# Performance work log

Hardware: AMD Instinct MI355X
Metric: run time of the kernel (lower is better)

## Reference

```python
import math
import jax, jax.numpy as jnp
from jax import lax
import numpy as np

WH, WW = 5, 9          # window_size
EH, EW = 3, 5          # expand_size = ((ws+1)//2)
NHEAD = 4
D = 512
PK, PS = 4, 4          # pool kernel / stride


def _valid_ind_rolled():
    m = np.ones((4, WH, WW), dtype=np.float32)
    m[0, :WH - EH, :WW - EW] = 0  # tl
    m[1, :WH - EH, EW:] = 0       # tr
    m[2, EH:, :WW - EW] = 0       # bl
    m[3, EH:, EW:] = 0            # br
    return np.nonzero(m.reshape(-1))[0]

VALID_IND = jnp.asarray(_valid_ind_rolled())  # (148,)


def _forward(x, masks, Wq, bq, Wk, bk, Wv, bv, Wp, bp, pool_w, pool_b):
    b, t, h, w, c = x.shape
    hd = c // NHEAD
    n_wh, n_ww = h // WH, w // WW
    n_win = n_wh * n_ww
    S = WH * WW  # tokens per window per frame (45)

    q = x @ Wq + bq
    k = x @ Wk + bk
    v = x @ Wv + bv

    def wp(a):  # window partition -> (b, n_win, nhead, t, S, hd)
        a = a.reshape(b, t, n_wh, WH, n_ww, WW, NHEAD, hd)
        a = a.transpose(0, 2, 4, 6, 1, 3, 5, 7)
        return a.reshape(b, n_win, NHEAD, t, S, hd)

    win_q, win_k, win_v = wp(q), wp(k), wp(v)

    # rolled (shifted) windows, gathered by the static valid-index buffer
    shifts = ((-EH, -EW), (-EH, EW), (EH, -EW), (EH, EW))
    roll_k = jnp.concatenate([wp(jnp.roll(k, s, axis=(2, 3))) for s in shifts], axis=4)[:, :, :, :, VALID_IND]
    roll_v = jnp.concatenate([wp(jnp.roll(v, s, axis=(2, 3))) for s in shifts], axis=4)[:, :, :, :, VALID_IND]

    # pooled global tokens via depthwise conv (kernel 4, stride 4)
    px = lax.conv_general_dilated(
        x.reshape(b * t, h, w, c), pool_w, (PS, PS), 'VALID',
        dimension_numbers=('NHWC', 'HWIO', 'NHWC'), feature_group_count=c) + pool_b
    ph, pw = px.shape[1], px.shape[2]
    P = ph * pw
    px = px.reshape(b, t, P, c)

    def pool_tok(a):  # (b,t,P,c) -> (b,1,nhead,t,P,hd)
        return a.reshape(b, t, P, NHEAD, hd).transpose(0, 3, 1, 2, 4)[:, None]

    pk = jnp.broadcast_to(pool_tok(px @ Wk + bk), (b, n_win, NHEAD, t, P, hd))
    pv = jnp.broadcast_to(pool_tok(px @ Wv + bv), (b, n_win, NHEAD, t, P, hd))

    win_k_full = jnp.concatenate([win_k, roll_k, pk], axis=4)  # (b,n_win,nh,t,K,hd)
    win_v_full = jnp.concatenate([win_v, roll_v, pv], axis=4)
    K = win_k_full.shape[4]

    # window-level mask: max-pool per window per frame, summed over frames, >0
    wmask = masks[..., 0].reshape(b, t, n_wh, WH, n_ww, WW).max(axis=(3, 5))
    wmask = wmask.reshape(b, t, n_win).sum(axis=1) > 0  # (b, n_win)

    scale = 1.0 / math.sqrt(hd)

    # dense spatiotemporal attention (used for masked windows)
    qd = win_q.reshape(b, n_win, NHEAD, t * S, hd)
    kd = win_k_full.reshape(b, n_win, NHEAD, t * K, hd)
    vd = win_v_full.reshape(b, n_win, NHEAD, t * K, hd)
    att_d = jax.nn.softmax(jnp.einsum('bnhqd,bnhkd->bnhqk', qd, kd) * scale, axis=-1)
    y_d = jnp.einsum('bnhqk,bnhkd->bnhqd', att_d, vd).reshape(b, n_win, NHEAD, t, S, hd)

    # per-frame local window attention (used for unmasked windows; keys = first S = window tokens)
    att_l = jax.nn.softmax(jnp.einsum('bnhtqd,bnhtkd->bnhtqk', win_q, win_k) * scale, axis=-1)
    y_l = jnp.einsum('bnhtqk,bnhtkd->bnhtqd', att_l, win_v)

    out = jnp.where(wmask[:, :, None, None, None, None], y_d, y_l)
    out = out.reshape(b, n_wh, n_ww, NHEAD, t, WH, WW, hd)
    out = out.transpose(0, 4, 1, 5, 2, 6, 3, 7).reshape(b, t, h, w, c)
    return out @ Wp + bp


def setup_inputs() -> dict:
    key = jax.random.key(0)
    ks = jax.random.split(key, 8)
    b, t, h, w = 1, 6, 40, 72
    x = jax.random.normal(ks[0], (b, t, h, w, D), dtype=jnp.float32)
    wm = (jax.random.uniform(ks[1], (b, t, h // WH, w // WW)) < 0.3).astype(jnp.float32)
    masks = jnp.repeat(jnp.repeat(wm, WH, axis=2), WW, axis=3)[..., None]
    s = 0.02

    def lin(kk):
        k1, k2 = jax.random.split(kk)
        return (jax.random.normal(k1, (D, D), jnp.float32) * s,
                jax.random.normal(k2, (D,), jnp.float32) * s)

    Wq, bq = lin(ks[2])
    Wk, bk = lin(ks[3])
    Wv, bv = lin(ks[4])
    Wp, bp = lin(ks[5])
    pool_w = jax.random.normal(ks[6], (PK, PK, 1, D), jnp.float32) * s
    pool_b = jax.random.normal(ks[7], (D,), jnp.float32) * s
    return {'x': x, 'masks': masks, 'Wq': Wq, 'bq': bq, 'Wk': Wk, 'bk': bk,
            'Wv': Wv, 'bv': bv, 'Wp': Wp, 'bp': bp, 'pool_w': pool_w, 'pool_b': pool_b}


def reference(x, masks, Wq, bq, Wk, bk, Wv, bv, Wp, bp, pool_w, pool_b):
    return _forward(x, masks, Wq, bq, Wk, bk, Wv, bv, Wp, bp, pool_w, pool_b)
```

## Files before the change

kernel.cpp:

```cpp
#include <hip/hip_runtime.h>

typedef unsigned short u16;
typedef unsigned int u32;
typedef __bf16 bf16x8 __attribute__((ext_vector_type(8)));
typedef float f32x4 __attribute__((ext_vector_type(4)));

#define TT 6
#define NTOK (6*40*72)
#define KTOT 373
#define NKEYS (TT*KTOT)
#define NCH2 35
#define SCALE 0.08838834764831845f
#define K_EXP2 0.12751743f

__device__ __forceinline__ float bf2f(u16 u){ u32 x = ((u32)u) << 16; return __builtin_bit_cast(float, x); }
__device__ __forceinline__ u16 f2bf(float f){ return __builtin_bit_cast(u16, (__bf16)f); }

__device__ __forceinline__ void gload16(const u16* g, u16* l){
  __builtin_amdgcn_global_load_lds(
      (const __attribute__((address_space(1))) void*)g,
      (__attribute__((address_space(3))) void*)l, 16, 0, 0);
}

__global__ __launch_bounds__(256) void convert_x(const float* __restrict__ src, u16* __restrict__ dst, int n4)
{
  int i = blockIdx.x * 256 + threadIdx.x;
  if (i >= n4) return;
  float4 v = *(const float4*)(src + (size_t)i * 4);
  u16 o[4] = {f2bf(v.x), f2bf(v.y), f2bf(v.z), f2bf(v.w)};
  *(uint2*)(dst + (size_t)i * 4) = *(const uint2*)o;
}

__global__ __launch_bounds__(256) void transpose_w(
    const float* __restrict__ w0, const float* __restrict__ w1,
    const float* __restrict__ w2, const float* __restrict__ w3, u16* __restrict__ out)
{
  __shared__ float tile[64][65];
  int m = blockIdx.z;
  const float* src = m == 0 ? w0 : (m == 1 ? w1 : (m == 2 ? w2 : w3));
  int kb = blockIdx.x * 64, nb = blockIdx.y * 64;
  int tid = threadIdx.x;
  int tx = tid & 63, ty = tid >> 6;
#pragma unroll
  for (int i = 0; i < 16; i++)
    tile[ty + 4*i][tx] = src[(size_t)(kb + ty + 4*i) * 512 + nb + tx];
  __syncthreads();
#pragma unroll
  for (int i = 0; i < 16; i++)
    out[m * 262144 + (size_t)(nb + ty + 4*i) * 512 + kb + tx] = f2bf(tile[tx][ty + 4*i]);
}

__global__ __launch_bounds__(256) void gemm_bias(
    const u16* __restrict__ A, const u16* __restrict__ wt,
    const float* __restrict__ b0, const float* __restrict__ b1, const float* __restrict__ b2,
    u16* __restrict__ c0, u16* __restrict__ c1, u16* __restrict__ c2, float* __restrict__ cf,
    int wo0, int wo1, int wo2, int M)
{
  __shared__ __align__(16) u16 sA[128*32];
  __shared__ __align__(16) u16 sB[128*32];
  int z = blockIdx.z;
  const u16* Bt = wt + (size_t)(z == 0 ? wo0 : (z == 1 ? wo1 : wo2)) * 262144;
  const float* bias = z == 0 ? b0 : (z == 1 ? b1 : b2);
  u16* Cout = z == 0 ? c0 : (z == 1 ? c1 : c2);
  int mbase = blockIdx.x * 128, nbase = blockIdx.y * 128;
  int tid = threadIdx.x, lane = tid & 63, wave = tid >> 6;
  int wm = (wave >> 1) * 64, wn = (wave & 1) * 64;
  int quad = lane >> 4, tr = lane & 15;
  int lrow = lane >> 2;
  int seg  = (lane & 3) ^ (lrow & 3);

  const u16* gA[2]; const u16* gB[2];
#pragma unroll
  for (int r = 0; r < 2; r++){
    gA[r] = A  + (size_t)(mbase + wave*32 + r*16 + lrow) * 512 + seg*8;
    gB[r] = Bt + (size_t)(nbase + wave*32 + r*16 + lrow) * 512 + seg*8;
  }
  u16* lA[2]; u16* lB[2];
#pragma unroll
  for (int r = 0; r < 2; r++){
    lA[r] = &sA[(wave*32 + r*16) * 32];
    lB[r] = &sB[(wave*32 + r*16) * 32];
  }

  f32x4 acc[4][4];
#pragma unroll
  for (int i = 0; i < 4; i++)
#pragma unroll
    for (int j = 0; j < 4; j++){ acc[i][j][0]=0.f; acc[i][j][1]=0.f; acc[i][j][2]=0.f; acc[i][j][3]=0.f; }

  int rcol = (quad ^ (tr & 3)) * 8;

  for (int k0 = 0; k0 < 512; k0 += 32){
    if (k0) __syncthreads();
#pragma unroll
    for (int r = 0; r < 2; r++){
      gload16(gA[r] + k0, lA[r]);
      gload16(gB[r] + k0, lB[r]);
    }
    __syncthreads();
    bf16x8 a[4], b[4];
#pragma unroll
    for (int i = 0; i < 4; i++) a[i] = *(const bf16x8*)(&sA[(wm + i*16 + tr)*32 + rcol]);
#pragma unroll
    for (int j = 0; j < 4; j++) b[j] = *(const bf16x8*)(&sB[(wn + j*16 + tr)*32 + rcol]);
#pragma unroll
    for (int i = 0; i < 4; i++)
#pragma unroll
      for (int j = 0; j < 4; j++)
        acc[i][j] = __builtin_amdgcn_mfma_f32_16x16x32_bf16(a[i], b[j], acc[i][j], 0, 0, 0);
  }

#pragma unroll
  for (int j = 0; j < 4; j++){
    int col = nbase + wn + j*16 + tr;
    float bv = bias[col];
#pragma unroll
    for (int i = 0; i < 4; i++)
#pragma unroll
      for (int r2 = 0; r2 < 4; r2++){
        int row = mbase + wm + i*16 + quad*4 + r2;
        if (row < M){
          float val = acc[i][j][r2] + bv;
          if (cf) cf[(size_t)row * 512 + col] = val;
          else    Cout[(size_t)row * 512 + col] = f2bf(val);
        }
      }
  }
}

__global__ __launch_bounds__(256) void pool_conv(
    const float* __restrict__ x, const float* __restrict__ pw,
    const float* __restrict__ pb, u16* __restrict__ px)
{
  int idx = blockIdx.x * 256 + threadIdx.x;
  int c = idx & 511, n = idx >> 9;
  int f = n / 180, rp = n % 180, ph = rp / 18, pwc = rp % 18;
  float acc = pb[c];
#pragma unroll
  for (int i = 0; i < 4; i++)
#pragma unroll
    for (int j = 0; j < 4; j++){
      int hh = ph*4 + i, ww = pwc*4 + j;
      acc += x[((size_t)((f*40 + hh)*72 + ww)) * 512 + c] * pw[(i*4 + j)*512 + c];
    }
  px[idx] = f2bf(acc);
}

__global__ void prep(const float* __restrict__ masks, int* __restrict__ wmask, int* __restrict__ vi)
{
  int tid = threadIdx.x;
  if (tid < 64) wmask[tid] = 0;
  __syncthreads();
  if (tid < 384){
    int f = tid / 64, win = tid & 63;
    int wi = win >> 3, wj = win & 7;
    int flag = 0;
    for (int p = 0; p < 45; p++){
      int hh = wi*5 + p/9, ww = wj*9 + p%9;
      if (masks[(f*40 + hh)*72 + ww] > 0.f) flag = 1;
    }
    if (flag) atomicOr(&wmask[win], 1);
  }
  if (tid == 448){
    int cnt = 0;
    for (int e = 0; e < 180; e++){
      int s = e / 45, pos = e % 45, pr = pos / 9, pc = pos % 9;
      bool inval = (s == 0 && pr < 2 && pc < 4) || (s == 1 && pr < 2 && pc >= 5) ||
                   (s == 2 && pr >= 3 && pc < 4) || (s == 3 && pr >= 3 && pc >= 5);
      if (!inval) vi[cnt++] = e;
    }
  }
}

__global__ __launch_bounds__(256) void build_idx(const int* __restrict__ vip, int* __restrict__ idxTab)
{
  int win = blockIdx.x, wi = win >> 3, wj = win & 7;
  for (int i = threadIdx.x; i < NKEYS; i += 256){
    int f = i / KTOT, slot = i - f * KTOT;
    int idx;
    if (slot < 45){
      int hh = wi*5 + slot/9, ww = wj*9 + slot%9;
      idx = ((f*40 + hh)*72 + ww) * 1024;
    } else if (slot < 193){
      int e = vip[slot - 45];
      int s2 = e / 45, pos = e - s2*45, pr = pos/9, pc = pos - pr*9;
      int hh = wi*5 + pr + ((s2 < 2) ? 3 : -3);
      int ww = wj*9 + pc + ((s2 & 1) ? -5 : 5);
      if (hh < 0) hh += 40; else if (hh >= 40) hh -= 40;
      if (ww < 0) ww += 72; else if (ww >= 72) ww -= 72;
      idx = ((f*40 + hh)*72 + ww) * 1024;
    } else {
      idx = ~((f*180 + (slot - 193)) * 1024);
    }
    idxTab[win * 2240 + i] = idx;
  }
}

__global__ __launch_bounds__(512) void attn_dense(
    const u16* __restrict__ qb, const u16* __restrict__ kb, const u16* __restrict__ vb,
    const u16* __restrict__ pkb, const u16* __restrict__ pvb,
    const int* __restrict__ wmaskp, const int* __restrict__ idxTab,
    u16* __restrict__ yb)
{
  __shared__ __align__(16) u16 sK[64][136];
  __shared__ __align__(16) u16 sVt[128][72];
  __shared__ __align__(16) u16 sP[288][72];
  __shared__ int sIdx[2240];
  __shared__ float sDenX[32];

  int win = blockIdx.x, head = blockIdx.y;
  if (!wmaskp[win]) return;
  int wi = win >> 3, wj = win & 7;
  int tid = threadIdx.x, lane = tid & 63, wave = tid >> 6;
  int quad = lane >> 4, tr = lane & 15;

  if (tid < 32) sDenX[tid] = 0.f;
  {
    const int* g = idxTab + win * 2240;
    for (int i = tid; i < NKEYS; i += 512) sIdx[i] = g[i];
  }

  int mts[3] = {2*wave, 2*wave + 1, 16 + (wave >> 2)};
  bf16x8 qf[3][4];
#pragma unroll
  for (int im = 0; im < 3; im++){
    int row = mts[im]*16 + tr;
    int f = row / 48, r = row - f*48;
    bool vld = r < 45;
    int hh = wi*5 + r/9, ww = wj*9 + r%9;
    const u16* qp = qb + ((size_t)((f*40 + hh)*72 + ww))*512 + head*128;
#pragma unroll
    for (int kt = 0; kt < 4; kt++){
      uint4 v = make_uint4(0,0,0,0);
      if (vld) v = *(const uint4*)(qp + kt*32 + quad*8);
      qf[im][kt] = __builtin_bit_cast(bf16x8, v);
    }
  }

  f32x4 accv[2][8], accx[2];
#pragma unroll
  for (int m = 0; m < 2; m++)
#pragma unroll
    for (int nt = 0; nt < 8; nt++){ accv[m][nt][0]=0.f; accv[m][nt][1]=0.f; accv[m][nt][2]=0.f; accv[m][nt][3]=0.f; }
  accx[0][0]=0.f; accx[0][1]=0.f; accx[0][2]=0.f; accx[0][3]=0.f;
  accx[1][0]=0.f; accx[1][1]=0.f; accx[1][2]=0.f; accx[1][3]=0.f;
  float dacc[2][4], daccx[4];
#pragma unroll
  for (int m = 0; m < 2; m++)
#pragma unroll
    for (int r2 = 0; r2 < 4; r2++) dacc[m][r2] = 0.f;
#pragma unroll
  for (int r2 = 0; r2 < 4; r2++) daccx[r2] = 0.f;

  __syncthreads();

  const char* kb2  = (const char*)kb  + head*256 + (tid & 15)*16;
  const char* pkb2 = (const char*)pkb + head*256 + (tid & 15)*16;
  const char* vb2  = (const char*)vb  + head*256 + (tid >> 6)*16;
  const char* pvb2 = (const char*)pvb + head*256 + (tid >> 6)*16;

  uint4 pfk[2], pfv[2];
  auto pref = [&](int ch){
#pragma unroll
    for (int r = 0; r < 2; r++){ pfk[r] = make_uint4(0,0,0,0); pfv[r] = make_uint4(0,0,0,0); }
    if (ch < NCH2){
      int base = ch * 64;
#pragma unroll
      for (int r = 0; r < 2; r++){
        int jg = base + (tid >> 4) + 32*r;
        if (jg < NKEYS){
          int off = sIdx[jg];
          pfk[r] = *(const uint4*)(off >= 0 ? kb2 + off : pkb2 + ~off);
        }
      }
      int jgv = base + (tid & 63);
      if (jgv < NKEYS){
        int off = sIdx[jgv];
        const char* src = (off >= 0) ? vb2 + off : pvb2 + ~off;
#pragma unroll
        for (int r = 0; r < 2; r++)
          pfv[r] = *(const uint4*)(src + r*128);
      }
    }
  };
  pref(0);

  for (int ch = 0; ch < NCH2; ch++){
    __syncthreads();
#pragma unroll
    for (int r = 0; r < 2; r++)
      *(uint4*)(&sK[(tid >> 4) + 32*r][(tid & 15)*8]) = pfk[r];
    {
      int keyv = tid & 63;
#pragma unroll
      for (int r = 0; r < 2; r++){
        int dgv = (tid >> 6) + 8*r;
        u32 vv[4] = {pfv[r].x, pfv[r].y, pfv[r].z, pfv[r].w};
#pragma unroll
        for (int q2 = 0; q2 < 4; q2++){
          sVt[dgv*8 + q2*2][keyv]     = (u16)(vv[q2] & 0xffff);
          sVt[dgv*8 + q2*2 + 1][keyv] = (u16)(vv[q2] >> 16);
        }
      }
    }
    __syncthreads();
    pref(ch + 1);

#pragma unroll
    for (int nt = 0; nt < 4; nt++){
      bf16x8 bk[4];
#pragma unroll
      for (int kt = 0; kt < 4; kt++) bk[kt] = *(const bf16x8*)(&sK[nt*16 + tr][kt*32 + quad*8]);
      int colg = ch*64 + nt*16 + tr;
      bool vld = colg < NKEYS;
#pragma unroll
      for (int m = 0; m < 2; m++){
        f32x4 s = {0.f, 0.f, 0.f, 0.f};
#pragma unroll
        for (int kt = 0; kt < 4; kt++) s = __builtin_amdgcn_mfma_f32_16x16x32_bf16(qf[m][kt], bk[kt], s, 0, 0, 0);
        int mt = 2*wave + m;
#pragma unroll
        for (int r2 = 0; r2 < 4; r2++){
          float p = vld ? __builtin_amdgcn_exp2f(s[r2] * K_EXP2) : 0.f;
          sP[mt*16 + quad*4 + r2][nt*16 + tr] = f2bf(p);
          dacc[m][r2] += p;
        }
      }
      if (nt == (wave & 3)){
        f32x4 s = {0.f, 0.f, 0.f, 0.f};
#pragma unroll
        for (int kt = 0; kt < 4; kt++) s = __builtin_amdgcn_mfma_f32_16x16x32_bf16(qf[2][kt], bk[kt], s, 0, 0, 0);
        int e = 16 + (wave >> 2);
#pragma unroll
        for (int r2 = 0; r2 < 4; r2++){
          float p = vld ? __builtin_amdgcn_exp2f(s[r2] * K_EXP2) : 0.f;
          sP[e*16 + quad*4 + r2][nt*16 + tr] = f2bf(p);
          daccx[r2] += p;
        }
      }
    }
    __syncthreads();

#pragma unroll
    for (int kt2 = 0; kt2 < 2; kt2++){
      bf16x8 a0 = *(const bf16x8*)(&sP[(2*wave)*16 + tr][kt2*32 + quad*8]);
      bf16x8 a1 = *(const bf16x8*)(&sP[(2*wave + 1)*16 + tr][kt2*32 + quad*8]);
      bf16x8 ax = *(const bf16x8*)(&sP[(16 + (wave >> 2))*16 + tr][kt2*32 + quad*8]);
#pragma unroll
      for (int nt = 0; nt < 8; nt++){
        bf16x8 bv = *(const bf16x8*)(&sVt[nt*16 + tr][kt2*32 + quad*8]);
        accv[0][nt] = __builtin_amdgcn_mfma_f32_16x16x32_bf16(a0, bv, accv[0][nt], 0, 0, 0);
        accv[1][nt] = __builtin_amdgcn_mfma_f32_16x16x32_bf16(a1, bv, accv[1][nt], 0, 0, 0);
      }
      int he0 = (wave & 3)*2;
      bf16x8 bx0 = *(const bf16x8*)(&sVt[he0*16 + tr][kt2*32 + quad*8]);
      bf16x8 bx1 = *(const bf16x8*)(&sVt[(he0+1)*16 + tr][kt2*32 + quad*8]);
      accx[0] = __builtin_amdgcn_mfma_f32_16x16x32_bf16(ax, bx0, accx[0], 0, 0, 0);
      accx[1] = __builtin_amdgcn_mfma_f32_16x16x32_bf16(ax, bx1, accx[1], 0, 0, 0);
    }
  }

#pragma unroll
  for (int r2 = 0; r2 < 4; r2++){
    float d = daccx[r2];
    d += __shfl_xor(d, 1, 64); d += __shfl_xor(d, 2, 64);
    d += __shfl_xor(d, 4, 64); d += __shfl_xor(d, 8, 64);
    if (tr == 0) atomicAdd(&sDenX[(wave >> 2)*16 + quad*4 + r2], d);
  }
  __syncthreads();

#pragma unroll
  for (int m = 0; m < 2; m++){
#pragma unroll
    for (int r2 = 0; r2 < 4; r2++){
      float d = dacc[m][r2];
      d += __shfl_xor(d, 1, 64); d += __shfl_xor(d, 2, 64);
      d += __shfl_xor(d, 4, 64); d += __shfl_xor(d, 8, 64);
      float dinvv = 1.f / d;
      int row = (2*wave + m)*16 + quad*4 + r2;
      int f = row / 48, r = row - f*48;
      if (r < 45){
        int hh = wi*5 + r/9, ww = wj*9 + r%9;
        size_t base = ((size_t)((f*40 + hh)*72 + ww))*512 + head*128;
#pragma unroll
        for (int nt = 0; nt < 8; nt++)
          yb[base + nt*16 + tr] = f2bf(accv[m][nt][r2] * dinvv);
      }
    }
  }
  {
    int e = 16 + (wave >> 2), he0 = (wave & 3)*2;
#pragma unroll
    for (int r2 = 0; r2 < 4; r2++){
      int row = e*16 + quad*4 + r2;
      int f = row / 48, r = row - f*48;
      if (r < 45){
        float dinvv = 1.f / sDenX[(e - 16)*16 + quad*4 + r2];
        int hh = wi*5 + r/9, ww = wj*9 + r%9;
        size_t base = ((size_t)((f*40 + hh)*72 + ww))*512 + head*128;
        yb[base + he0*16 + tr]       = f2bf(accx[0][r2] * dinvv);
        yb[base + (he0 + 1)*16 + tr] = f2bf(accx[1][r2] * dinvv);
      }
    }
  }
}

__device__ __forceinline__ const u16* key_src_local(int slot, int qf, int wi, int wj, int head,
    const u16* __restrict__ tokbuf)
{
  int hh = wi*5 + slot/9, ww = wj*9 + slot%9;
  return tokbuf + ((size_t)((qf*40 + hh)*72 + ww)) * 512 + head * 128;
}

__global__ __launch_bounds__(256) void attn_local(
    const u16* __restrict__ qb, const u16* __restrict__ kb, const u16* __restrict__ vb,
    const int* __restrict__ wmaskp, u16* __restrict__ yb)
{
  __shared__ __align__(16) u16 sQ[48][136];
  __shared__ __align__(16) u16 sK[64][136];
  __shared__ __align__(16) u16 sVt[128][72];
  __shared__ __align__(16) u16 sP[48][72];
  __shared__ float sDen[48];

  int win = blockIdx.x, head = blockIdx.y, qf = blockIdx.z;
  if (wmaskp[win]) return;
  int wi = win >> 3, wj = win & 7;
  int tid = threadIdx.x, lane = tid & 63, wave = tid >> 6;
  int quad = lane >> 4, tr = lane & 15;

  if (tid < 48) sDen[tid] = 0.f;

#pragma unroll
  for (int r = 0; r < 3; r++){
    int u = tid + 256 * r;
    int row = u >> 4, dg = u & 15;
    uint4 val = make_uint4(0,0,0,0);
    if (row < 45){
      int hh = wi*5 + row/9, ww = wj*9 + row%9;
      val = *(const uint4*)(qb + ((size_t)((qf*40 + hh)*72 + ww)) * 512 + head*128 + dg*8);
    }
    *(uint4*)(&sQ[row][dg * 8]) = val;
  }

  const int nkeys = 45;
  f32x4 acc[3][2];
#pragma unroll
  for (int a = 0; a < 3; a++)
#pragma unroll
    for (int b = 0; b < 2; b++){ acc[a][b][0]=0.f; acc[a][b][1]=0.f; acc[a][b][2]=0.f; acc[a][b][3]=0.f; }

#pragma unroll
  for (int r = 0; r < 4; r++){
    int u = tid + 256 * r;
    int key = u >> 4, dg = u & 15;
    uint4 val = make_uint4(0,0,0,0);
    if (key < nkeys) val = *(const uint4*)(key_src_local(key, qf, wi, wj, head, kb) + dg * 8);
    *(uint4*)(&sK[key][dg * 8]) = val;
  }
#pragma unroll
  for (int r = 0; r < 4; r++){
    int u = tid + 256 * r;
    int key = u & 63, dg = u >> 6;
    uint4 val = make_uint4(0,0,0,0);
    if (key < nkeys) val = *(const uint4*)(key_src_local(key, qf, wi, wj, head, vb) + dg * 8);
    u32 vv[4] = {val.x, val.y, val.z, val.w};
#pragma unroll
    for (int q2 = 0; q2 < 4; q2++){
      sVt[dg*8 + q2*2][key]     = (u16)(vv[q2] & 0xffff);
      sVt[dg*8 + q2*2 + 1][key] = (u16)(vv[q2] >> 16);
    }
  }
  __syncthreads();

#pragma unroll
  for (int mt = 0; mt < 3; mt++){
    f32x4 sacc = {0.f, 0.f, 0.f, 0.f};
#pragma unroll
    for (int kt = 0; kt < 4; kt++){
      bf16x8 a = *(const bf16x8*)(&sQ[mt*16 + tr][kt*32 + quad*8]);
      bf16x8 b = *(const bf16x8*)(&sK[wave*16 + tr][kt*32 + quad*8]);
      sacc = __builtin_amdgcn_mfma_f32_16x16x32_bf16(a, b, sacc, 0, 0, 0);
    }
    int colg = wave * 16 + tr;
    float pr4[4];
#pragma unroll
    for (int r2 = 0; r2 < 4; r2++){
      float p = (colg < nkeys) ? __builtin_amdgcn_exp2f(sacc[r2] * K_EXP2) : 0.f;
      sP[mt*16 + quad*4 + r2][wave*16 + tr] = f2bf(p);
      pr4[r2] = p;
    }
#pragma unroll
    for (int r2 = 0; r2 < 4; r2++){
      float ps = pr4[r2];
      ps += __shfl_xor(ps, 1, 64);
      ps += __shfl_xor(ps, 2, 64);
      ps += __shfl_xor(ps, 4, 64);
      ps += __shfl_xor(ps, 8, 64);
      if (tr == 0) atomicAdd(&sDen[mt*16 + quad*4 + r2], ps);
    }
  }
  __syncthreads();

#pragma unroll
  for (int mt = 0; mt < 3; mt++)
#pragma unroll
    for (int nt = 0; nt < 2; nt++)
#pragma unroll
      for (int kt = 0; kt < 2; kt++){
        bf16x8 a = *(const bf16x8*)(&sP[mt*16 + tr][kt*32 + quad*8]);
        bf16x8 b = *(const bf16x8*)(&sVt[wave*32 + nt*16 + tr][kt*32 + quad*8]);
        acc[mt][nt] = __builtin_amdgcn_mfma_f32_16x16x32_bf16(a, b, acc[mt][nt], 0, 0, 0);
      }
  __syncthreads();

#pragma unroll
  for (int mt = 0; mt < 3; mt++)
#pragma unroll
    for (int r2 = 0; r2 < 4; r2++){
      int row = mt*16 + quad*4 + r2;
      if (row < 45){
        float dinv = 1.0f / sDen[row];
        int hh = wi*5 + row/9, ww = wj*9 + row%9;
        size_t base = ((size_t)((qf*40 + hh)*72 + ww)) * 512 + head * 128;
#pragma unroll
        for (int nt = 0; nt < 2; nt++){
          int col = wave*32 + nt*16 + tr;
          yb[base + col] = f2bf(acc[mt][nt][r2] * dinv);
        }
      }
    }
}

extern "C" void kernel_launch(void* const* d_in, const int* in_sizes, int n_in,
                              void* d_out, int out_size, void* d_ws, size_t ws_size,
                              hipStream_t stream)
{
  const float* x     = (const float*)d_in[0];
  const float* masks = (const float*)d_in[1];
  const float* Wq = (const float*)d_in[2];  const float* bq = (const float*)d_in[3];
  const float* Wk = (const float*)d_in[4];  const float* bk = (const float*)d_in[5];
  const float* Wv = (const float*)d_in[6];  const float* bv = (const float*)d_in[7];
  const float* Wp = (const float*)d_in[8];  const float* bp = (const float*)d_in[9];
  const float* pw = (const float*)d_in[10]; const float* pb = (const float*)d_in[11];
  float* out = (float*)d_out;

  char* ws = (char*)d_ws;
  size_t off = 0;
  auto alloc = [&](size_t bytes) -> char* {
    char* p = ws + off; off += (bytes + 255) & ~(size_t)255; return p;
  };
  u16* wt    = (u16*)alloc((size_t)4 * 512 * 512 * 2);
  u16* xbf   = (u16*)alloc((size_t)NTOK * 512 * 2);
  u16* qbuf  = (u16*)alloc((size_t)NTOK * 512 * 2);
  u16* kbuf  = (u16*)alloc((size_t)NTOK * 512 * 2);
  u16* vbuf  = (u16*)alloc((size_t)NTOK * 512 * 2);
  u16* pxbuf = (u16*)alloc((size_t)1080 * 512 * 2);
  u16* pkbuf = (u16*)alloc((size_t)1080 * 512 * 2);
  u16* pvbuf = (u16*)alloc((size_t)1080 * 512 * 2);
  u16* ybuf  = (u16*)alloc((size_t)NTOK * 512 * 2);
  int* wmaskb = (int*)alloc(64 * 4);
  int* vib    = (int*)alloc(148 * 4);
  int* idxTabb = (int*)alloc((size_t)64 * 2240 * 4);

  convert_x<<<dim3((NTOK*512/4 + 255)/256), 256, 0, stream>>>(x, xbf, NTOK*512/4);
  transpose_w<<<dim3(8, 8, 4), 256, 0, stream>>>(Wq, Wk, Wv, Wp, wt);
  gemm_bias<<<dim3(135, 4, 3), 256, 0, stream>>>(xbf, wt, bq, bk, bv, qbuf, kbuf, vbuf, nullptr, 0, 1, 2, NTOK);
  pool_conv<<<dim3(2160), 256, 0, stream>>>(x, pw, pb, pxbuf);
  gemm_bias<<<dim3(9, 4, 2), 256, 0, stream>>>(pxbuf, wt, bk, bv, bv, pkbuf, pvbuf, pvbuf, nullptr, 1, 2, 2, 1080);
  prep<<<dim3(1), 512, 0, stream>>>(masks, wmaskb, vib);
  build_idx<<<dim3(64), 256, 0, stream>>>(vib, idxTabb);
  attn_dense<<<dim3(64, 4), 512, 0, stream>>>(qbuf, kbuf, vbuf, pkbuf, pvbuf, wmaskb, idxTabb, ybuf);
  attn_local<<<dim3(64, 4, 6), 256, 0, stream>>>(qbuf, kbuf, vbuf, wmaskb, ybuf);
  gemm_bias<<<dim3(135, 4, 1), 256, 0, stream>>>(ybuf, wt, bp, bp, bp, nullptr, nullptr, nullptr, out, 3, 3, 3, NTOK);
}
```

Baseline: 394.1 us.

## Split dense window attention query rows across two 256-thread blocks

The dense attention kernel is relaunched with a grid z-dimension of 2, and each 256-thread block handles half of the 18 query tiles (9 each) instead of one 512-thread block handling all of them. The aim is to double the number of blocks for the roughly 30% of active windows, improving CU occupancy and cutting shared memory per block. In exchange, the gathered K/V chunks for each window and head are loaded and transposed twice, once per half, which doubles that global traffic.

```diff
diff --git a/kernel.cpp b/kernel.cpp
--- a/kernel.cpp
+++ b/kernel.cpp
@@ -196,7 +196,7 @@
   }
 }
 
-__global__ __launch_bounds__(512) void attn_dense(
+__global__ __launch_bounds__(256) void attn_dense(
     const u16* __restrict__ qb, const u16* __restrict__ kb, const u16* __restrict__ vb,
     const u16* __restrict__ pkb, const u16* __restrict__ pvb,
     const int* __restrict__ wmaskp, const int* __restrict__ idxTab,
@@ -204,23 +204,24 @@
 {
   __shared__ __align__(16) u16 sK[64][136];
   __shared__ __align__(16) u16 sVt[128][72];
-  __shared__ __align__(16) u16 sP[288][72];
+  __shared__ __align__(16) u16 sP[144][72];
   __shared__ int sIdx[2240];
-  __shared__ float sDenX[32];
-
-  int win = blockIdx.x, head = blockIdx.y;
+  __shared__ float sDenX[16];
+
+  int win = blockIdx.x, head = blockIdx.y, half = blockIdx.z;
   if (!wmaskp[win]) return;
   int wi = win >> 3, wj = win & 7;
   int tid = threadIdx.x, lane = tid & 63, wave = tid >> 6;
   int quad = lane >> 4, tr = lane & 15;
-
-  if (tid < 32) sDenX[tid] = 0.f;
+  int mtb = half * 9;
+
+  if (tid < 16) sDenX[tid] = 0.f;
   {
     const int* g = idxTab + win * 2240;
-    for (int i = tid; i < NKEYS; i += 512) sIdx[i] = g[i];
-  }
-
-  int mts[3] = {2*wave, 2*wave + 1, 16 + (wave >> 2)};
+    for (int i = tid; i < NKEYS; i += 256) sIdx[i] = g[i];
+  }
+
+  int mts[3] = {mtb + 2*wave, mtb + 2*wave + 1, mtb + 8};
   bf16x8 qf[3][4];
 #pragma unroll
   for (int im = 0; im < 3; im++){
@@ -259,15 +260,15 @@
   const char* vb2  = (const char*)vb  + head*256 + (tid >> 6)*16;
   const char* pvb2 = (const char*)pvb + head*256 + (tid >> 6)*16;
 
-  uint4 pfk[2], pfv[2];
+  uint4 pfk[4], pfv[4];
   auto pref = [&](int ch){
 #pragma unroll
-    for (int r = 0; r < 2; r++){ pfk[r] = make_uint4(0,0,0,0); pfv[r] = make_uint4(0,0,0,0); }
+    for (int r = 0; r < 4; r++){ pfk[r] = make_uint4(0,0,0,0); pfv[r] = make_uint4(0,0,0,0); }
     if (ch < NCH2){
       int base = ch * 64;
 #pragma unroll
-      for (int r = 0; r < 2; r++){
-        int jg = base + (tid >> 4) + 32*r;
+      for (int r = 0; r < 4; r++){
+        int jg = base + (tid >> 4) + 16*r;
         if (jg < NKEYS){
           int off = sIdx[jg];
           pfk[r] = *(const uint4*)(off >= 0 ? kb2 + off : pkb2 + ~off);
@@ -278,8 +279,8 @@
         int off = sIdx[jgv];
         const char* src = (off >= 0) ? vb2 + off : pvb2 + ~off;
 #pragma unroll
-        for (int r = 0; r < 2; r++)
-          pfv[r] = *(const uint4*)(src + r*128);
+        for (int r = 0; r < 4; r++)
+          pfv[r] = *(const uint4*)(src + r*64);
       }
     }
   };
@@ -288,13 +289,13 @@
   for (int ch = 0; ch < NCH2; ch++){
     __syncthreads();
 #pragma unroll
-    for (int r = 0; r < 2; r++)
-      *(uint4*)(&sK[(tid >> 4) + 32*r][(tid & 15)*8]) = pfk[r];
+    for (int r = 0; r < 4; r++)
+      *(uint4*)(&sK[(tid >> 4) + 16*r][(tid & 15)*8]) = pfk[r];
     {
       int keyv = tid & 63;
 #pragma unroll
-      for (int r = 0; r < 2; r++){
-        int dgv = (tid >> 6) + 8*r;
+      for (int r = 0; r < 4; r++){
+        int dgv = (tid >> 6) + 4*r;
         u32 vv[4] = {pfv[r].x, pfv[r].y, pfv[r].z, pfv[r].w};
 #pragma unroll
         for (int q2 = 0; q2 < 4; q2++){
@@ -318,23 +319,22 @@
         f32x4 s = {0.f, 0.f, 0.f, 0.f};
 #pragma unroll
         for (int kt = 0; kt < 4; kt++) s = __builtin_amdgcn_mfma_f32_16x16x32_bf16(qf[m][kt], bk[kt], s, 0, 0, 0);
-        int mt = 2*wave + m;
+        int lm = 2*wave + m;
 #pragma unroll
         for (int r2 = 0; r2 < 4; r2++){
           float p = vld ? __builtin_amdgcn_exp2f(s[r2] * K_EXP2) : 0.f;
-          sP[mt*16 + quad*4 + r2][nt*16 + tr] = f2bf(p);
+          sP[lm*16 + quad*4 + r2][nt*16 + tr] = f2bf(p);
           dacc[m][r2] += p;
         }
       }
-      if (nt == (wave & 3)){
+      if (nt == wave){
         f32x4 s = {0.f, 0.f, 0.f, 0.f};
 #pragma unroll
         for (int kt = 0; kt < 4; kt++) s = __builtin_amdgcn_mfma_f32_16x16x32_bf16(qf[2][kt], bk[kt], s, 0, 0, 0);
-        int e = 16 + (wave >> 2);
 #pragma unroll
         for (int r2 = 0; r2 < 4; r2++){
           float p = vld ? __builtin_amdgcn_exp2f(s[r2] * K_EXP2) : 0.f;
-          sP[e*16 + quad*4 + r2][nt*16 + tr] = f2bf(p);
+          sP[128 + quad*4 + r2][nt*16 + tr] = f2bf(p);
           daccx[r2] += p;
         }
       }
@@ -345,14 +345,14 @@
     for (int kt2 = 0; kt2 < 2; kt2++){
       bf16x8 a0 = *(const bf16x8*)(&sP[(2*wave)*16 + tr][kt2*32 + quad*8]);
       bf16x8 a1 = *(const bf16x8*)(&sP[(2*wave + 1)*16 + tr][kt2*32 + quad*8]);
-      bf16x8 ax = *(const bf16x8*)(&sP[(16 + (wave >> 2))*16 + tr][kt2*32 + quad*8]);
+      bf16x8 ax = *(const bf16x8*)(&sP[128 + tr][kt2*32 + quad*8]);
 #pragma unroll
       for (int nt = 0; nt < 8; nt++){
         bf16x8 bv = *(const bf16x8*)(&sVt[nt*16 + tr][kt2*32 + quad*8]);
         accv[0][nt] = __builtin_amdgcn_mfma_f32_16x16x32_bf16(a0, bv, accv[0][nt], 0, 0, 0);
         accv[1][nt] = __builtin_amdgcn_mfma_f32_16x16x32_bf16(a1, bv, accv[1][nt], 0, 0, 0);
       }
-      int he0 = (wave & 3)*2;
+      int he0 = wave*2;
       bf16x8 bx0 = *(const bf16x8*)(&sVt[he0*16 + tr][kt2*32 + quad*8]);
       bf16x8 bx1 = *(const bf16x8*)(&sVt[(he0+1)*16 + tr][kt2*32 + quad*8]);
       accx[0] = __builtin_amdgcn_mfma_f32_16x16x32_bf16(ax, bx0, accx[0], 0, 0, 0);
@@ -365,7 +365,7 @@
     float d = daccx[r2];
     d += __shfl_xor(d, 1, 64); d += __shfl_xor(d, 2, 64);
     d += __shfl_xor(d, 4, 64); d += __shfl_xor(d, 8, 64);
-    if (tr == 0) atomicAdd(&sDenX[(wave >> 2)*16 + quad*4 + r2], d);
+    if (tr == 0) atomicAdd(&sDenX[quad*4 + r2], d);
   }
   __syncthreads();
 
@@ -377,7 +377,7 @@
       d += __shfl_xor(d, 1, 64); d += __shfl_xor(d, 2, 64);
       d += __shfl_xor(d, 4, 64); d += __shfl_xor(d, 8, 64);
       float dinvv = 1.f / d;
-      int row = (2*wave + m)*16 + quad*4 + r2;
+      int row = (mtb + 2*wave + m)*16 + quad*4 + r2;
       int f = row / 48, r = row - f*48;
       if (r < 45){
         int hh = wi*5 + r/9, ww = wj*9 + r%9;
@@ -389,13 +389,13 @@
     }
   }
   {
-    int e = 16 + (wave >> 2), he0 = (wave & 3)*2;
+    int he0 = wave*2;
 #pragma unroll
     for (int r2 = 0; r2 < 4; r2++){
-      int row = e*16 + quad*4 + r2;
+      int row = (mtb + 8)*16 + quad*4 + r2;
       int f = row / 48, r = row - f*48;
       if (r < 45){
-        float dinvv = 1.f / sDenX[(e - 16)*16 + quad*4 + r2];
+        float dinvv = 1.f / sDenX[quad*4 + r2];
         int hh = wi*5 + r/9, ww = wj*9 + r%9;
         size_t base = ((size_t)((f*40 + hh)*72 + ww))*512 + head*128;
         yb[base + he0*16 + tr]       = f2bf(accx[0][r2] * dinvv);
@@ -569,7 +569,7 @@
   gemm_bias<<<dim3(9, 4, 2), 256, 0, stream>>>(pxbuf, wt, bk, bv, bv, pkbuf, pvbuf, pvbuf, nullptr, 1, 2, 2, 1080);
   prep<<<dim3(1), 512, 0, stream>>>(masks, wmaskb, vib);
   build_idx<<<dim3(64), 256, 0, stream>>>(vib, idxTabb);
-  attn_dense<<<dim3(64, 4), 512, 0, stream>>>(qbuf, kbuf, vbuf, pkbuf, pvbuf, wmaskb, idxTabb, ybuf);
+  attn_dense<<<dim3(64, 4, 2), 256, 0, stream>>>(qbuf, kbuf, vbuf, pkbuf, pvbuf, wmaskb, idxTabb, ybuf);
   attn_local<<<dim3(64, 4, 6), 256, 0, stream>>>(qbuf, kbuf, vbuf, wmaskb, ybuf);
   gemm_bias<<<dim3(135, 4, 1), 256, 0, stream>>>(ybuf, wt, bp, bp, bp, nullptr, nullptr, nullptr, out, 3, 3, 3, NTOK);
 }
```

New measurement: 467.8 us. 18.7% more time.

## Transpose score MFMA and pack P/V^T stores as 32-bit words in LDS

Applied to the files above, without the earlier changes.

Swaps the MFMA operand order for QK^T so each lane holds four consecutive keys of one query row. The bf16 probabilities can then be packed into one 64-bit LDS store instead of four scattered 16-bit stores. The V transpose is reorganised so each thread loads two adjacent keys and writes packed 32-bit words into sVt. Row-sum reduction shrinks to one accumulator per tile, combined by cross-quad shuffles and then broadcast. The aim is fewer LDS store instructions and bank conflicts, at the cost of a more intricate index mapping that must stay consistent with the PV MFMA operand layout.

```diff
diff --git a/kernel.cpp b/kernel.cpp
--- a/kernel.cpp
+++ b/kernel.cpp
@@ -204,7 +204,7 @@
 {
   __shared__ __align__(16) u16 sK[64][136];
   __shared__ __align__(16) u16 sVt[128][72];
-  __shared__ __align__(16) u16 sP[288][72];
+  __shared__ __align__(16) u32 sPw[288][36];
   __shared__ int sIdx[2240];
   __shared__ float sDenX[32];
 
@@ -244,20 +244,16 @@
     for (int nt = 0; nt < 8; nt++){ accv[m][nt][0]=0.f; accv[m][nt][1]=0.f; accv[m][nt][2]=0.f; accv[m][nt][3]=0.f; }
   accx[0][0]=0.f; accx[0][1]=0.f; accx[0][2]=0.f; accx[0][3]=0.f;
   accx[1][0]=0.f; accx[1][1]=0.f; accx[1][2]=0.f; accx[1][3]=0.f;
-  float dacc[2][4], daccx[4];
-#pragma unroll
-  for (int m = 0; m < 2; m++)
-#pragma unroll
-    for (int r2 = 0; r2 < 4; r2++) dacc[m][r2] = 0.f;
-#pragma unroll
-  for (int r2 = 0; r2 < 4; r2++) daccx[r2] = 0.f;
-
-  __syncthreads();
-
+  float dacc[2] = {0.f, 0.f};
+  float daccx = 0.f;
+
+  __syncthreads();
+
+  int upair = tid & 31, dgv = tid >> 5;
   const char* kb2  = (const char*)kb  + head*256 + (tid & 15)*16;
   const char* pkb2 = (const char*)pkb + head*256 + (tid & 15)*16;
-  const char* vb2  = (const char*)vb  + head*256 + (tid >> 6)*16;
-  const char* pvb2 = (const char*)pvb + head*256 + (tid >> 6)*16;
+  const char* vb2  = (const char*)vb  + head*256 + dgv*16;
+  const char* pvb2 = (const char*)pvb + head*256 + dgv*16;
 
   uint4 pfk[2], pfv[2];
   auto pref = [&](int ch){
@@ -273,13 +269,13 @@
           pfk[r] = *(const uint4*)(off >= 0 ? kb2 + off : pkb2 + ~off);
         }
       }
-      int jgv = base + (tid & 63);
-      if (jgv < NKEYS){
-        int off = sIdx[jgv];
-        const char* src = (off >= 0) ? vb2 + off : pvb2 + ~off;
-#pragma unroll
-        for (int r = 0; r < 2; r++)
-          pfv[r] = *(const uint4*)(src + r*128);
+#pragma unroll
+      for (int r = 0; r < 2; r++){
+        int jg = base + 2*upair + r;
+        if (jg < NKEYS){
+          int off = sIdx[jg];
+          pfv[r] = *(const uint4*)(off >= 0 ? vb2 + off : pvb2 + ~off);
+        }
       }
     }
   };
@@ -291,16 +287,13 @@
     for (int r = 0; r < 2; r++)
       *(uint4*)(&sK[(tid >> 4) + 32*r][(tid & 15)*8]) = pfk[r];
     {
-      int keyv = tid & 63;
-#pragma unroll
-      for (int r = 0; r < 2; r++){
-        int dgv = (tid >> 6) + 8*r;
-        u32 vv[4] = {pfv[r].x, pfv[r].y, pfv[r].z, pfv[r].w};
-#pragma unroll
-        for (int q2 = 0; q2 < 4; q2++){
-          sVt[dgv*8 + q2*2][keyv]     = (u16)(vv[q2] & 0xffff);
-          sVt[dgv*8 + q2*2 + 1][keyv] = (u16)(vv[q2] >> 16);
-        }
+      u32 va[4] = {pfv[0].x, pfv[0].y, pfv[0].z, pfv[0].w};
+      u32 vbp[4] = {pfv[1].x, pfv[1].y, pfv[1].z, pfv[1].w};
+#pragma unroll
+      for (int jj = 0; jj < 8; jj++){
+        u32 lo = (va[jj >> 1] >> (16*(jj & 1))) & 0xffffu;
+        u32 hi = (vbp[jj >> 1] >> (16*(jj & 1))) & 0xffffu;
+        ((u32*)&sVt[dgv*8 + jj][0])[upair] = lo | (hi << 16);
       }
     }
     __syncthreads();
@@ -311,41 +304,46 @@
       bf16x8 bk[4];
 #pragma unroll
       for (int kt = 0; kt < 4; kt++) bk[kt] = *(const bf16x8*)(&sK[nt*16 + tr][kt*32 + quad*8]);
-      int colg = ch*64 + nt*16 + tr;
-      bool vld = colg < NKEYS;
+      int colb = ch*64 + nt*16 + quad*4;
 #pragma unroll
       for (int m = 0; m < 2; m++){
         f32x4 s = {0.f, 0.f, 0.f, 0.f};
 #pragma unroll
-        for (int kt = 0; kt < 4; kt++) s = __builtin_amdgcn_mfma_f32_16x16x32_bf16(qf[m][kt], bk[kt], s, 0, 0, 0);
-        int mt = 2*wave + m;
+        for (int kt = 0; kt < 4; kt++) s = __builtin_amdgcn_mfma_f32_16x16x32_bf16(bk[kt], qf[m][kt], s, 0, 0, 0);
+        float p[4];
 #pragma unroll
         for (int r2 = 0; r2 < 4; r2++){
-          float p = vld ? __builtin_amdgcn_exp2f(s[r2] * K_EXP2) : 0.f;
-          sP[mt*16 + quad*4 + r2][nt*16 + tr] = f2bf(p);
-          dacc[m][r2] += p;
+          p[r2] = (colb + r2 < NKEYS) ? __builtin_amdgcn_exp2f(s[r2] * K_EXP2) : 0.f;
+          dacc[m] += p[r2];
         }
+        uint2 w;
+        w.x = (u32)f2bf(p[0]) | ((u32)f2bf(p[1]) << 16);
+        w.y = (u32)f2bf(p[2]) | ((u32)f2bf(p[3]) << 16);
+        *(uint2*)(&sPw[(2*wave + m)*16 + tr][nt*8 + quad*2]) = w;
       }
       if (nt == (wave & 3)){
         f32x4 s = {0.f, 0.f, 0.f, 0.f};
 #pragma unroll
-        for (int kt = 0; kt < 4; kt++) s = __builtin_amdgcn_mfma_f32_16x16x32_bf16(qf[2][kt], bk[kt], s, 0, 0, 0);
-        int e = 16 + (wave >> 2);
+        for (int kt = 0; kt < 4; kt++) s = __builtin_amdgcn_mfma_f32_16x16x32_bf16(bk[kt], qf[2][kt], s, 0, 0, 0);
+        float p[4];
 #pragma unroll
         for (int r2 = 0; r2 < 4; r2++){
-          float p = vld ? __builtin_amdgcn_exp2f(s[r2] * K_EXP2) : 0.f;
-          sP[e*16 + quad*4 + r2][nt*16 + tr] = f2bf(p);
-          daccx[r2] += p;
+          p[r2] = (colb + r2 < NKEYS) ? __builtin_amdgcn_exp2f(s[r2] * K_EXP2) : 0.f;
+          daccx += p[r2];
         }
+        uint2 w;
+        w.x = (u32)f2bf(p[0]) | ((u32)f2bf(p[1]) << 16);
+        w.y = (u32)f2bf(p[2]) | ((u32)f2bf(p[3]) << 16);
+        *(uint2*)(&sPw[(16 + (wave >> 2))*16 + tr][nt*8 + quad*2]) = w;
       }
     }
     __syncthreads();
 
 #pragma unroll
     for (int kt2 = 0; kt2 < 2; kt2++){
-      bf16x8 a0 = *(const bf16x8*)(&sP[(2*wave)*16 + tr][kt2*32 + quad*8]);
-      bf16x8 a1 = *(const bf16x8*)(&sP[(2*wave + 1)*16 + tr][kt2*32 + quad*8]);
-      bf16x8 ax = *(const bf16x8*)(&sP[(16 + (wave >> 2))*16 + tr][kt2*32 + quad*8]);
+      bf16x8 a0 = *(const bf16x8*)(&sPw[(2*wave)*16 + tr][kt2*16 + quad*4]);
+      bf16x8 a1 = *(const bf16x8*)(&sPw[(2*wave + 1)*16 + tr][kt2*16 + quad*4]);
+      bf16x8 ax = *(const bf16x8*)(&sPw[(16 + (wave >> 2))*16 + tr][kt2*16 + quad*4]);
 #pragma unroll
       for (int nt = 0; nt < 8; nt++){
         bf16x8 bv = *(const bf16x8*)(&sVt[nt*16 + tr][kt2*32 + quad*8]);
@@ -360,23 +358,25 @@
     }
   }
 
-#pragma unroll
-  for (int r2 = 0; r2 < 4; r2++){
-    float d = daccx[r2];
-    d += __shfl_xor(d, 1, 64); d += __shfl_xor(d, 2, 64);
-    d += __shfl_xor(d, 4, 64); d += __shfl_xor(d, 8, 64);
-    if (tr == 0) atomicAdd(&sDenX[(wave >> 2)*16 + quad*4 + r2], d);
-  }
-  __syncthreads();
-
+  float dred[2];
 #pragma unroll
   for (int m = 0; m < 2; m++){
+    float d = dacc[m];
+    d += __shfl_xor(d, 16, 64); d += __shfl_xor(d, 32, 64);
+    dred[m] = d;
+  }
+  {
+    float d = daccx;
+    d += __shfl_xor(d, 16, 64); d += __shfl_xor(d, 32, 64);
+    if (lane < 16) atomicAdd(&sDenX[(wave >> 2)*16 + lane], d);
+  }
+  __syncthreads();
+
+#pragma unroll
+  for (int m = 0; m < 2; m++){
 #pragma unroll
     for (int r2 = 0; r2 < 4; r2++){
-      float d = dacc[m][r2];
-      d += __shfl_xor(d, 1, 64); d += __shfl_xor(d, 2, 64);
-      d += __shfl_xor(d, 4, 64); d += __shfl_xor(d, 8, 64);
-      float dinvv = 1.f / d;
+      float dinvv = 1.f / __shfl(dred[m], quad*4 + r2, 64);
       int row = (2*wave + m)*16 + quad*4 + r2;
       int f = row / 48, r = row - f*48;
       if (r < 45){
```

Measured after the change: 386.1 us. -2.0%, faster.
